# Kernel optimization log

Measured on AMD Instinct MI355X. Metric: run time of the kernel, lower is better.

Reference implementation:

```python
import jax, jax.numpy as jnp
import numpy as np

WS = 8                 # window size (attn_grid_window_size)
N_WIN = WS * WS        # tokens per window = 64
EPS_LN = 1e-5

def _rel_index():
    # standard Swin/MaxViT relative position index for an 8x8 window
    coords = np.stack(np.meshgrid(np.arange(WS), np.arange(WS), indexing='ij')).reshape(2, -1)
    rel = coords[:, :, None] - coords[:, None, :]
    rel = rel.transpose(1, 2, 0).astype(np.int32)
    rel[..., 0] += WS - 1
    rel[..., 1] += WS - 1
    rel[..., 0] *= 2 * WS - 1
    return rel.sum(-1)  # [N_WIN, N_WIN] in [0, (2*WS-1)^2)

def layernorm(x, g, b):
    m = jnp.mean(x, -1, keepdims=True)
    v = jnp.mean((x - m) ** 2, -1, keepdims=True)
    return (x - m) * jax.lax.rsqrt(v + EPS_LN) * g + b

def l2norm(x):
    n = jnp.sqrt(jnp.sum(x * x, -1, keepdims=True))
    return x / jnp.maximum(n, 1e-12)  # torch F.normalize semantics

def setup_inputs() -> dict:
    key = jax.random.key(0)
    ks = jax.random.split(key, 4)
    B, C, H, W = 2, 256, 256, 256
    heads = 16
    s = 0.02
    return dict(
        X=jax.random.normal(ks[0], (B, C, H, W), jnp.float32),
        pre_g=jnp.ones((C,), jnp.float32), pre_b=jnp.zeros((C,), jnp.float32),
        post_g=jnp.ones((C,), jnp.float32), post_b=jnp.zeros((C,), jnp.float32),
        qkv_w=jax.random.normal(ks[1], (C, 3 * C), jnp.float32) * s,
        qkv_b=jnp.zeros((3 * C,), jnp.float32),
        proj_w=jax.random.normal(ks[2], (C, C), jnp.float32) * s,
        proj_b=jnp.zeros((C,), jnp.float32),
        rel_bias_table=jax.random.normal(ks[3], ((2 * WS - 1) ** 2, heads), jnp.float32) * s,
        rel_index=jnp.asarray(_rel_index()),
    )

def reference(X, pre_g, pre_b, post_g, post_b, qkv_w, qkv_b, proj_w, proj_b, rel_bias_table, rel_index):
    B, C, H, W = X.shape
    heads = rel_bias_table.shape[1]
    hd = C // heads
    # block partition: [B, C, H, W] -> [B*nH*nW, WS*WS, C]
    xw = X.reshape(B, C, H // WS, WS, W // WS, WS).transpose(0, 2, 4, 3, 5, 1)
    xw = xw.reshape(-1, N_WIN, C)
    Bw = xw.shape[0]
    # pre-norm + relative self-attention
    xn = layernorm(xw, pre_g, pre_b)
    qkv = (xn @ qkv_w + qkv_b).reshape(Bw, N_WIN, 3, heads, hd).transpose(2, 0, 3, 1, 4)
    q, k, v = qkv[0], qkv[1], qkv[2]            # [Bw, h, N, hd]
    q = l2norm(q)
    k = l2norm(k)                               # use_normalised_qk=True (MetNet-3)
    bias = rel_bias_table[rel_index.reshape(-1)].reshape(N_WIN, N_WIN, heads).transpose(2, 0, 1)
    attn = jax.nn.softmax(jnp.einsum('bhnd,bhmd->bhnm', q, k) + bias[None], axis=-1)
    out = jnp.einsum('bhnm,bhmd->bhnd', attn, v).transpose(0, 2, 1, 3).reshape(Bw, N_WIN, C)
    out = out @ proj_w + proj_b
    # residual, then post-norm branch (mlp = Identity)
    x = xw + out
    x = x + layernorm(x, post_g, post_b)
    # reverse partition -> [B, C, H, W]
    x = x.reshape(B, H // WS, W // WS, WS, WS, C).transpose(0, 5, 1, 3, 2, 4).reshape(B, C, H, W)
    return x
```

## Files before the change

### kernel.cpp

```cpp
#include <hip/hip_runtime.h>
#include <stdint.h>

typedef unsigned short u16;
typedef unsigned int   u32;

typedef short s8v __attribute__((ext_vector_type(8)));
typedef short s4v __attribute__((ext_vector_type(4)));
typedef float f4v __attribute__((ext_vector_type(4)));

struct __align__(8) US4 { u16 x, y, z, w; };

__device__ __forceinline__ u16 f2bf(float f) {
    union { float f; u32 u; } v; v.f = f;
    u32 u = v.u;
    return (u16)((u + 0x7fffu + ((u >> 16) & 1u)) >> 16);
}

#define MFMA16(a, b, c) __builtin_amdgcn_mfma_f32_16x16x16bf16_1k((a), (b), (c), 0, 0, 0)
#define MFMA32(a, b, c) __builtin_amdgcn_mfma_f32_16x16x32_bf16((a), (b), (c), 0, 0, 0)

__global__ void pack_kernel(const float* __restrict__ qkv_w, const float* __restrict__ proj_w,
                            const float* __restrict__ table, const int* __restrict__ ridx,
                            u16* __restrict__ pkQ, u16* __restrict__ pkP, float* __restrict__ biasP)
{
    int tid = blockIdx.x * 256 + threadIdx.x;
    if (tid < 24576) {
        int g = tid;
        int lane = g & 63, ks = (g >> 6) & 7, mt = g >> 9;
        int quad = lane >> 4, c = lane & 15;
        union { u16 h[8]; s8v v; } tmp;
#pragma unroll
        for (int j = 0; j < 8; ++j) {
            int kk = ks * 32 + quad * 8 + j;
            tmp.h[j] = f2bf(qkv_w[kk * 768 + mt * 16 + c]);
        }
        *(s8v*)&pkQ[g * 8] = tmp.v;
    } else if (tid < 32768) {
        int g = tid - 24576;
        int lane = g & 63, ks = (g >> 6) & 7, mt = g >> 9;
        int quad = lane >> 4, c = lane & 15;
        union { u16 h[8]; s8v v; } tmp;
#pragma unroll
        for (int j = 0; j < 8; ++j) {
            int kk = ks * 32 + quad * 8 + j;
            tmp.h[j] = f2bf(proj_w[kk * 256 + mt * 16 + c]);
        }
        *(s8v*)&pkP[g * 8] = tmp.v;
    } else if (tid < 49152) {
        int g = tid - 32768;
        int h = g >> 10, rest = (g >> 6) & 15, lane = g & 63;
        int mt = rest >> 2, nt = rest & 3;
        int quad = lane >> 4, c = lane & 15;
        int query = nt * 16 + c;
#pragma unroll
        for (int r = 0; r < 4; ++r) {
            int key = mt * 16 + quad * 4 + r;
            biasP[g * 4 + r] = table[ridx[query * 64 + key] * 16 + h];
        }
    }
}

__global__ __launch_bounds__(1024)
void attn_win_kernel(const float* __restrict__ X,
                     const float* __restrict__ pre_g, const float* __restrict__ pre_b,
                     const float* __restrict__ post_g, const float* __restrict__ post_b,
                     const float* __restrict__ qkv_b, const float* __restrict__ proj_b,
                     const u16* __restrict__ pkQ, const u16* __restrict__ pkP,
                     const float* __restrict__ biasP,
                     float* __restrict__ out)
{
    __shared__ __align__(16) unsigned char smem[138752];
    u16*   xnS = (u16*)smem;
    u16*   qS  = xnS + 16896;
    u16*   kS  = qS + 16896;
    u16*   vS  = kS + 16896;
    float* xf  = (float*)(smem + 67584);
    float* st  = (float*)(smem + 138240);

    const int tid  = threadIdx.x;
    const int w    = tid >> 6;
    const int l    = tid & 63;
    const int quad = l >> 4;
    const int c    = l & 15;

    const int win = blockIdx.x;
    const int bb = win >> 10;
    const int wh = (win >> 5) & 31;
    const int ww = win & 31;
    const size_t base = (((size_t)bb * 256) * 256 + wh * 8) * 256 + ww * 8;

    f4v xreg[4];
    {
        const int ch0 = (tid >> 4);
        const int t0  = (tid & 15) * 4;
        const int r0 = t0 >> 3, c0 = t0 & 7;
#pragma unroll
        for (int it = 0; it < 4; ++it) {
            int ch = it * 64 + ch0;
            f4v v = *(const f4v*)(X + base + (size_t)ch * 65536 + r0 * 256 + c0);
            xreg[it] = v;
            *(f4v*)&xf[ch * 68 + t0] = v;
        }
    }
    __syncthreads();

    {
        int tk = w * 4 + quad;
        float s = 0.f, ss = 0.f;
#pragma unroll
        for (int j = 0; j < 16; ++j) {
            float x = xf[(c + 16 * j) * 68 + tk];
            s += x; ss += x * x;
        }
#pragma unroll
        for (int m = 1; m < 16; m <<= 1) { s += __shfl_xor(s, m, 64); ss += __shfl_xor(ss, m, 64); }
        float mean = s * (1.f / 256.f);
        float var  = ss * (1.f / 256.f) - mean * mean;
        float rstd = rsqrtf(var + 1e-5f);
        if (c == 0) { st[tk * 2] = mean; st[tk * 2 + 1] = rstd; }
    }
    __syncthreads();

    {
        int t = l;
        int chg = w * 16;
        float mean = st[t * 2], rstd = st[t * 2 + 1];
        union { u16 h[16]; s8v v[2]; } tmp;
#pragma unroll
        for (int j = 0; j < 16; ++j) {
            int ch = chg + j;
            float x = xf[ch * 68 + t];
            tmp.h[j] = f2bf((x - mean) * rstd * pre_g[ch] + pre_b[ch]);
        }
        *(s8v*)&xnS[t * 264 + chg]     = tmp.v[0];
        *(s8v*)&xnS[t * 264 + chg + 8] = tmp.v[1];
    }
    __syncthreads();

    {
        f4v acc[3][4];
#pragma unroll
        for (int i = 0; i < 3; ++i)
#pragma unroll
            for (int nt = 0; nt < 4; ++nt) acc[i][nt] = 0.f;

        const s8v* A = (const s8v*)pkQ;
#pragma unroll
        for (int ks = 0; ks < 8; ++ks) {
            s8v bfr[4];
#pragma unroll
            for (int nt = 0; nt < 4; ++nt)
                bfr[nt] = *(const s8v*)&xnS[(nt * 16 + c) * 264 + ks * 32 + quad * 8];
#pragma unroll
            for (int i = 0; i < 3; ++i) {
                int mt = w * 3 + i;
                s8v afr = A[(mt * 8 + ks) * 64 + l];
#pragma unroll
                for (int nt = 0; nt < 4; ++nt)
                    acc[i][nt] = MFMA32(afr, bfr[nt], acc[i][nt]);
            }
        }
#pragma unroll
        for (int i = 0; i < 3; ++i) {
            int mt = w * 3 + i;
            float b0 = qkv_b[mt * 16 + quad * 4 + 0];
            float b1 = qkv_b[mt * 16 + quad * 4 + 1];
            float b2 = qkv_b[mt * 16 + quad * 4 + 2];
            float b3 = qkv_b[mt * 16 + quad * 4 + 3];
#pragma unroll
            for (int nt = 0; nt < 4; ++nt) {
                f4v a = acc[i][nt];
                a[0] += b0; a[1] += b1; a[2] += b2; a[3] += b3;
                int tok = nt * 16 + c;
                if (mt < 32) {
                    float ss = a[0]*a[0] + a[1]*a[1] + a[2]*a[2] + a[3]*a[3];
                    ss += __shfl_xor(ss, 16, 64);
                    ss += __shfl_xor(ss, 32, 64);
                    float inv = 1.0f / fmaxf(sqrtf(ss), 1e-12f);
                    US4 pk;
                    pk.x = f2bf(a[0] * inv); pk.y = f2bf(a[1] * inv);
                    pk.z = f2bf(a[2] * inv); pk.w = f2bf(a[3] * inv);
                    int off = tok * 264 + (mt & 15) * 16 + quad * 4;
                    if (mt < 16) *(US4*)&qS[off] = pk;
                    else         *(US4*)&kS[off] = pk;
                } else {
                    float p0 = __shfl_xor(a[0], 1, 64), p1 = __shfl_xor(a[1], 1, 64);
                    float p2 = __shfl_xor(a[2], 1, 64), p3 = __shfl_xor(a[3], 1, 64);
                    int chb = (mt - 32) * 16 + quad * 4;
                    if ((l & 1) == 0) {
                        *(u32*)&vS[(chb + 0) * 72 + tok] = (u32)f2bf(a[0]) | ((u32)f2bf(p0) << 16);
                        *(u32*)&vS[(chb + 1) * 72 + tok] = (u32)f2bf(a[1]) | ((u32)f2bf(p1) << 16);
                    } else {
                        *(u32*)&vS[(chb + 2) * 72 + tok - 1] = (u32)f2bf(p2) | ((u32)f2bf(a[2]) << 16);
                        *(u32*)&vS[(chb + 3) * 72 + tok - 1] = (u32)f2bf(p3) | ((u32)f2bf(a[3]) << 16);
                    }
                }
            }
        }
    }
    __syncthreads();

    {
        const int h = w;
        s4v kfr[4], vfr[4];
#pragma unroll
        for (int mt = 0; mt < 4; ++mt)
            kfr[mt] = *(const s4v*)&kS[(mt * 16 + c) * 264 + h * 16 + quad * 4];
#pragma unroll
        for (int kt = 0; kt < 4; ++kt)
            vfr[kt] = *(const s4v*)&vS[(h * 16 + c) * 72 + kt * 16 + quad * 4];

        const f4v* BP = (const f4v*)biasP;
#pragma unroll
        for (int half = 0; half < 2; ++half) {
            f4v sT[4][2];
#pragma unroll
            for (int nt2 = 0; nt2 < 2; ++nt2) {
                int nt = half * 2 + nt2;
                s4v qfr = *(const s4v*)&qS[(nt * 16 + c) * 264 + h * 16 + quad * 4];
#pragma unroll
                for (int mt = 0; mt < 4; ++mt) {
                    f4v bv = BP[(h * 16 + mt * 4 + nt) * 64 + l];
                    sT[mt][nt2] = MFMA16(kfr[mt], qfr, bv);
                }
            }
#pragma unroll
            for (int nt2 = 0; nt2 < 2; ++nt2) {
                int nt = half * 2 + nt2;
                float mx = -1e30f;
#pragma unroll
                for (int mt = 0; mt < 4; ++mt)
#pragma unroll
                    for (int r = 0; r < 4; ++r) mx = fmaxf(mx, sT[mt][nt2][r]);
                mx = fmaxf(mx, __shfl_xor(mx, 16, 64));
                mx = fmaxf(mx, __shfl_xor(mx, 32, 64));
                float p[16];
                float sum = 0.f;
#pragma unroll
                for (int mt = 0; mt < 4; ++mt)
#pragma unroll
                    for (int r = 0; r < 4; ++r) {
                        float e = __expf(sT[mt][nt2][r] - mx);
                        p[mt * 4 + r] = e; sum += e;
                    }
                sum += __shfl_xor(sum, 16, 64);
                sum += __shfl_xor(sum, 32, 64);
                float inv = 1.f / sum;
                f4v o = 0.f;
#pragma unroll
                for (int kt = 0; kt < 4; ++kt) {
                    s4v pv = { (short)f2bf(p[kt * 4 + 0] * inv), (short)f2bf(p[kt * 4 + 1] * inv),
                               (short)f2bf(p[kt * 4 + 2] * inv), (short)f2bf(p[kt * 4 + 3] * inv) };
                    o = MFMA16(vfr[kt], pv, o);
                }
                US4 ov; ov.x = f2bf(o[0]); ov.y = f2bf(o[1]); ov.z = f2bf(o[2]); ov.w = f2bf(o[3]);
                *(US4*)&xnS[(nt * 16 + c) * 264 + h * 16 + quad * 4] = ov;
            }
        }
    }
    __syncthreads();

    {
        f4v acc[4];
#pragma unroll
        for (int nt = 0; nt < 4; ++nt) acc[nt] = 0.f;
        const s8v* A = (const s8v*)pkP;
#pragma unroll
        for (int ks = 0; ks < 8; ++ks) {
            s8v afr = A[(w * 8 + ks) * 64 + l];
#pragma unroll
            for (int nt = 0; nt < 4; ++nt) {
                s8v bfr = *(const s8v*)&xnS[(nt * 16 + c) * 264 + ks * 32 + quad * 8];
                acc[nt] = MFMA32(afr, bfr, acc[nt]);
            }
        }
        float b0 = proj_b[w * 16 + quad * 4 + 0];
        float b1 = proj_b[w * 16 + quad * 4 + 1];
        float b2 = proj_b[w * 16 + quad * 4 + 2];
        float b3 = proj_b[w * 16 + quad * 4 + 3];
#pragma unroll
        for (int nt = 0; nt < 4; ++nt) {
            int tok = nt * 16 + c;
            int chb = w * 16 + quad * 4;
            xf[(chb + 0) * 68 + tok] = acc[nt][0] + b0;
            xf[(chb + 1) * 68 + tok] = acc[nt][1] + b1;
            xf[(chb + 2) * 68 + tok] = acc[nt][2] + b2;
            xf[(chb + 3) * 68 + tok] = acc[nt][3] + b3;
        }
    }
    __syncthreads();

    {
        const int ch0 = (tid >> 4);
        const int t0  = (tid & 15) * 4;
#pragma unroll
        for (int it = 0; it < 4; ++it) {
            int ch = it * 64 + ch0;
            f4v v = *(f4v*)&xf[ch * 68 + t0];
            v += xreg[it];
            *(f4v*)&xf[ch * 68 + t0] = v;
        }
    }
    __syncthreads();

    {
        int tk = w * 4 + quad;
        float s = 0.f, ss = 0.f;
#pragma unroll
        for (int j = 0; j < 16; ++j) {
            float x = xf[(c + 16 * j) * 68 + tk];
            s += x; ss += x * x;
        }
#pragma unroll
        for (int m = 1; m < 16; m <<= 1) { s += __shfl_xor(s, m, 64); ss += __shfl_xor(ss, m, 64); }
        float mean = s * (1.f / 256.f);
        float var  = ss * (1.f / 256.f) - mean * mean;
        float rstd = rsqrtf(var + 1e-5f);
        if (c == 0) { st[tk * 2] = mean; st[tk * 2 + 1] = rstd; }
    }
    __syncthreads();

    {
        const int ch0 = (tid >> 4);
        const int t0  = (tid & 15) * 4;
        const int r0 = t0 >> 3, c0 = t0 & 7;
#pragma unroll
        for (int it = 0; it < 4; ++it) {
            int ch = it * 64 + ch0;
            f4v x = *(f4v*)&xf[ch * 68 + t0];
            float g = post_g[ch], b = post_b[ch];
            f4v y;
#pragma unroll
            for (int j = 0; j < 4; ++j) {
                float mean = st[(t0 + j) * 2], rstd = st[(t0 + j) * 2 + 1];
                y[j] = x[j] + (x[j] - mean) * rstd * g + b;
            }
            *(f4v*)(out + base + (size_t)ch * 65536 + r0 * 256 + c0) = y;
        }
    }
}

extern "C" void kernel_launch(void* const* d_in, const int* in_sizes, int n_in,
                              void* d_out, int out_size, void* d_ws, size_t ws_size,
                              hipStream_t stream)
{
    const float* X      = (const float*)d_in[0];
    const float* pre_g  = (const float*)d_in[1];
    const float* pre_b  = (const float*)d_in[2];
    const float* post_g = (const float*)d_in[3];
    const float* post_b = (const float*)d_in[4];
    const float* qkv_w  = (const float*)d_in[5];
    const float* qkv_b  = (const float*)d_in[6];
    const float* proj_w = (const float*)d_in[7];
    const float* proj_b = (const float*)d_in[8];
    const float* table  = (const float*)d_in[9];
    const int*   ridx   = (const int*)d_in[10];

    u16*   pkQ   = (u16*)d_ws;
    u16*   pkP   = (u16*)((char*)d_ws + 393216);
    float* biasP = (float*)((char*)d_ws + 524288);

    pack_kernel<<<192, 256, 0, stream>>>(qkv_w, proj_w, table, ridx, pkQ, pkP, biasP);
    attn_win_kernel<<<2048, 1024, 0, stream>>>(X, pre_g, pre_b, post_g, post_b,
                                               qkv_b, proj_b, pkQ, pkP, biasP,
                                               (float*)d_out);
}
```

Measured before the change: 526.5 us.

## Restructure window attention to 512 threads with per-head register fusion and smaller LDS

```diff
diff --git a/kernel.cpp b/kernel.cpp
--- a/kernel.cpp
+++ b/kernel.cpp
@@ -60,7 +60,7 @@
     }
 }
 
-__global__ __launch_bounds__(1024)
+__global__ __launch_bounds__(512, 4)
 void attn_win_kernel(const float* __restrict__ X,
                      const float* __restrict__ pre_g, const float* __restrict__ pre_b,
                      const float* __restrict__ post_g, const float* __restrict__ post_b,
@@ -69,124 +69,174 @@
                      const float* __restrict__ biasP,
                      float* __restrict__ out)
 {
-    __shared__ __align__(16) unsigned char smem[138752];
+    __shared__ __align__(16) unsigned char smem[75264];
     u16*   xnS = (u16*)smem;
-    u16*   qS  = xnS + 16896;
-    u16*   kS  = qS + 16896;
-    u16*   vS  = kS + 16896;
-    float* xf  = (float*)(smem + 67584);
-    float* st  = (float*)(smem + 138240);
+    u16*   vS  = (u16*)(smem + 33792);
+    float* xf  = (float*)smem;
+    float* pst = (float*)(smem + 70656);
+    float* st  = (float*)(smem + 74752);
 
     const int tid  = threadIdx.x;
     const int w    = tid >> 6;
     const int l    = tid & 63;
     const int quad = l >> 4;
-    const int c    = l & 15;
-
-    const int win = blockIdx.x;
+    const int cc   = l & 15;
+
+    const int bidx = blockIdx.x;
+    const int win  = ((bidx & 7) << 8) | (bidx >> 3);
     const int bb = win >> 10;
     const int wh = (win >> 5) & 31;
     const int ww = win & 31;
     const size_t base = (((size_t)bb * 256) * 256 + wh * 8) * 256 + ww * 8;
 
-    f4v xreg[4];
-    {
-        const int ch0 = (tid >> 4);
-        const int t0  = (tid & 15) * 4;
-        const int r0 = t0 >> 3, c0 = t0 & 7;
-#pragma unroll
-        for (int it = 0; it < 4; ++it) {
-            int ch = it * 64 + ch0;
-            f4v v = *(const f4v*)(X + base + (size_t)ch * 65536 + r0 * 256 + c0);
-            xreg[it] = v;
-            *(f4v*)&xf[ch * 68 + t0] = v;
-        }
-    }
-    __syncthreads();
-
-    {
-        int tk = w * 4 + quad;
-        float s = 0.f, ss = 0.f;
-#pragma unroll
-        for (int j = 0; j < 16; ++j) {
-            float x = xf[(c + 16 * j) * 68 + tk];
-            s += x; ss += x * x;
-        }
-#pragma unroll
-        for (int m = 1; m < 16; m <<= 1) { s += __shfl_xor(s, m, 64); ss += __shfl_xor(ss, m, 64); }
-        float mean = s * (1.f / 256.f);
-        float var  = ss * (1.f / 256.f) - mean * mean;
-        float rstd = rsqrtf(var + 1e-5f);
-        if (c == 0) { st[tk * 2] = mean; st[tk * 2 + 1] = rstd; }
-    }
-    __syncthreads();
-
-    {
-        int t = l;
-        int chg = w * 16;
-        float mean = st[t * 2], rstd = st[t * 2 + 1];
-        union { u16 h[16]; s8v v[2]; } tmp;
-#pragma unroll
-        for (int j = 0; j < 16; ++j) {
-            int ch = chg + j;
-            float x = xf[ch * 68 + t];
-            tmp.h[j] = f2bf((x - mean) * rstd * pre_g[ch] + pre_b[ch]);
-        }
-        *(s8v*)&xnS[t * 264 + chg]     = tmp.v[0];
-        *(s8v*)&xnS[t * 264 + chg + 8] = tmp.v[1];
-    }
-    __syncthreads();
-
-    {
-        f4v acc[3][4];
-#pragma unroll
-        for (int i = 0; i < 3; ++i)
-#pragma unroll
-            for (int nt = 0; nt < 4; ++nt) acc[i][nt] = 0.f;
-
-        const s8v* A = (const s8v*)pkQ;
-#pragma unroll
-        for (int ks = 0; ks < 8; ++ks) {
-            s8v bfr[4];
-#pragma unroll
-            for (int nt = 0; nt < 4; ++nt)
-                bfr[nt] = *(const s8v*)&xnS[(nt * 16 + c) * 264 + ks * 32 + quad * 8];
-#pragma unroll
-            for (int i = 0; i < 3; ++i) {
-                int mt = w * 3 + i;
-                s8v afr = A[(mt * 8 + ks) * 64 + l];
+    const int ch0 = tid >> 4;
+    const int t0  = (tid & 15) * 4;
+    const int r0  = t0 >> 3, c0 = t0 & 7;
+
+    f4v xv[8];
+#pragma unroll
+    for (int it = 0; it < 8; ++it) {
+        int ch = it * 32 + ch0;
+        xv[it] = *(const f4v*)(X + base + (size_t)ch * 65536 + r0 * 256 + c0);
+    }
+
+    {
+        float s[4] = {0.f,0.f,0.f,0.f}, ss[4] = {0.f,0.f,0.f,0.f};
+#pragma unroll
+        for (int it = 0; it < 8; ++it)
+#pragma unroll
+            for (int j = 0; j < 4; ++j) { float x = xv[it][j]; s[j] += x; ss[j] += x * x; }
+#pragma unroll
+        for (int j = 0; j < 4; ++j) {
+            s[j]  += __shfl_xor(s[j], 16, 64);  s[j]  += __shfl_xor(s[j], 32, 64);
+            ss[j] += __shfl_xor(ss[j], 16, 64); ss[j] += __shfl_xor(ss[j], 32, 64);
+        }
+        if (quad == 0) {
+#pragma unroll
+            for (int j = 0; j < 4; ++j) {
+                pst[(w * 64 + t0 + j) * 2]     = s[j];
+                pst[(w * 64 + t0 + j) * 2 + 1] = ss[j];
+            }
+        }
+    }
+    __syncthreads();
+    if (tid < 64) {
+        float S = 0.f, SS = 0.f;
+#pragma unroll
+        for (int wv = 0; wv < 8; ++wv) {
+            S  += pst[(wv * 64 + tid) * 2];
+            SS += pst[(wv * 64 + tid) * 2 + 1];
+        }
+        float mean = S * (1.f / 256.f);
+        float var  = SS * (1.f / 256.f) - mean * mean;
+        st[tid * 2] = mean; st[tid * 2 + 1] = rsqrtf(var + 1e-5f);
+    }
+    __syncthreads();
+
+    {
+        float mean[4], rstd[4];
+#pragma unroll
+        for (int j = 0; j < 4; ++j) { mean[j] = st[(t0 + j) * 2]; rstd[j] = st[(t0 + j) * 2 + 1]; }
+#pragma unroll
+        for (int it = 0; it < 8; ++it) {
+            int ch = it * 32 + ch0;
+            float g = pre_g[ch], b = pre_b[ch];
+            u16 m0 = f2bf((xv[it][0] - mean[0]) * rstd[0] * g + b);
+            u16 m1 = f2bf((xv[it][1] - mean[1]) * rstd[1] * g + b);
+            u16 m2 = f2bf((xv[it][2] - mean[2]) * rstd[2] * g + b);
+            u16 m3 = f2bf((xv[it][3] - mean[3]) * rstd[3] * g + b);
+            u32 m01 = (u32)m0 | ((u32)m1 << 16);
+            u32 m23 = (u32)m2 | ((u32)m3 << 16);
+            u32 p01 = __shfl_xor(m01, 16, 64);
+            u32 p23 = __shfl_xor(m23, 16, 64);
+            if ((quad & 1) == 0) {
+                *(u32*)&xnS[(t0 + 0) * 264 + ch] = (m01 & 0xffffu) | ((p01 & 0xffffu) << 16);
+                *(u32*)&xnS[(t0 + 1) * 264 + ch] = (m01 >> 16)    | (p01 & 0xffff0000u);
+            } else {
+                *(u32*)&xnS[(t0 + 2) * 264 + ch - 1] = (p23 & 0xffffu) | ((m23 & 0xffffu) << 16);
+                *(u32*)&xnS[(t0 + 3) * 264 + ch - 1] = (p23 >> 16)    | (m23 & 0xffff0000u);
+            }
+        }
+    }
+    __syncthreads();
+
+    US4 outbuf[2][4];
+    const s8v* AQ = (const s8v*)pkQ;
+#pragma unroll
+    for (int hi = 0; hi < 2; ++hi) {
+        const int head = w * 2 + hi;
+        s4v qfr[4], kfr[4];
+        {
+            f4v acc0[4], acc1[4], acc2[4];
+#pragma unroll
+            for (int nt = 0; nt < 4; ++nt) { acc0[nt] = 0.f; acc1[nt] = 0.f; acc2[nt] = 0.f; }
+#pragma unroll
+            for (int ks = 0; ks < 8; ++ks) {
+                s8v bfr[4];
 #pragma unroll
                 for (int nt = 0; nt < 4; ++nt)
-                    acc[i][nt] = MFMA32(afr, bfr[nt], acc[i][nt]);
-            }
-        }
-#pragma unroll
-        for (int i = 0; i < 3; ++i) {
-            int mt = w * 3 + i;
-            float b0 = qkv_b[mt * 16 + quad * 4 + 0];
-            float b1 = qkv_b[mt * 16 + quad * 4 + 1];
-            float b2 = qkv_b[mt * 16 + quad * 4 + 2];
-            float b3 = qkv_b[mt * 16 + quad * 4 + 3];
-#pragma unroll
-            for (int nt = 0; nt < 4; ++nt) {
-                f4v a = acc[i][nt];
-                a[0] += b0; a[1] += b1; a[2] += b2; a[3] += b3;
-                int tok = nt * 16 + c;
-                if (mt < 32) {
-                    float ss = a[0]*a[0] + a[1]*a[1] + a[2]*a[2] + a[3]*a[3];
-                    ss += __shfl_xor(ss, 16, 64);
-                    ss += __shfl_xor(ss, 32, 64);
-                    float inv = 1.0f / fmaxf(sqrtf(ss), 1e-12f);
-                    US4 pk;
-                    pk.x = f2bf(a[0] * inv); pk.y = f2bf(a[1] * inv);
-                    pk.z = f2bf(a[2] * inv); pk.w = f2bf(a[3] * inv);
-                    int off = tok * 264 + (mt & 15) * 16 + quad * 4;
-                    if (mt < 16) *(US4*)&qS[off] = pk;
-                    else         *(US4*)&kS[off] = pk;
-                } else {
+                    bfr[nt] = *(const s8v*)&xnS[(nt * 16 + cc) * 264 + ks * 32 + quad * 8];
+                s8v a0 = AQ[((head     ) * 8 + ks) * 64 + l];
+                s8v a1 = AQ[((head + 16) * 8 + ks) * 64 + l];
+                s8v a2 = AQ[((head + 32) * 8 + ks) * 64 + l];
+#pragma unroll
+                for (int nt = 0; nt < 4; ++nt) {
+                    acc0[nt] = MFMA32(a0, bfr[nt], acc0[nt]);
+                    acc1[nt] = MFMA32(a1, bfr[nt], acc1[nt]);
+                    acc2[nt] = MFMA32(a2, bfr[nt], acc2[nt]);
+                }
+            }
+            {
+                float b0 = qkv_b[head * 16 + quad * 4 + 0];
+                float b1 = qkv_b[head * 16 + quad * 4 + 1];
+                float b2 = qkv_b[head * 16 + quad * 4 + 2];
+                float b3 = qkv_b[head * 16 + quad * 4 + 3];
+#pragma unroll
+                for (int nt = 0; nt < 4; ++nt) {
+                    f4v a = acc0[nt];
+                    a[0] += b0; a[1] += b1; a[2] += b2; a[3] += b3;
+                    float sq = a[0]*a[0] + a[1]*a[1] + a[2]*a[2] + a[3]*a[3];
+                    sq += __shfl_xor(sq, 16, 64);
+                    sq += __shfl_xor(sq, 32, 64);
+                    float inv = 1.0f / fmaxf(sqrtf(sq), 1e-12f);
+                    s4v f;
+                    f[0] = (short)f2bf(a[0] * inv); f[1] = (short)f2bf(a[1] * inv);
+                    f[2] = (short)f2bf(a[2] * inv); f[3] = (short)f2bf(a[3] * inv);
+                    qfr[nt] = f;
+                }
+            }
+            {
+                float b0 = qkv_b[(head + 16) * 16 + quad * 4 + 0];
+                float b1 = qkv_b[(head + 16) * 16 + quad * 4 + 1];
+                float b2 = qkv_b[(head + 16) * 16 + quad * 4 + 2];
+                float b3 = qkv_b[(head + 16) * 16 + quad * 4 + 3];
+#pragma unroll
+                for (int nt = 0; nt < 4; ++nt) {
+                    f4v a = acc1[nt];
+                    a[0] += b0; a[1] += b1; a[2] += b2; a[3] += b3;
+                    float sq = a[0]*a[0] + a[1]*a[1] + a[2]*a[2] + a[3]*a[3];
+                    sq += __shfl_xor(sq, 16, 64);
+                    sq += __shfl_xor(sq, 32, 64);
+                    float inv = 1.0f / fmaxf(sqrtf(sq), 1e-12f);
+                    s4v f;
+                    f[0] = (short)f2bf(a[0] * inv); f[1] = (short)f2bf(a[1] * inv);
+                    f[2] = (short)f2bf(a[2] * inv); f[3] = (short)f2bf(a[3] * inv);
+                    kfr[nt] = f;
+                }
+            }
+            {
+                float b0 = qkv_b[(head + 32) * 16 + quad * 4 + 0];
+                float b1 = qkv_b[(head + 32) * 16 + quad * 4 + 1];
+                float b2 = qkv_b[(head + 32) * 16 + quad * 4 + 2];
+                float b3 = qkv_b[(head + 32) * 16 + quad * 4 + 3];
+                int chb = head * 16 + quad * 4;
+#pragma unroll
+                for (int nt = 0; nt < 4; ++nt) {
+                    f4v a = acc2[nt];
+                    a[0] += b0; a[1] += b1; a[2] += b2; a[3] += b3;
+                    int tok = nt * 16 + cc;
                     float p0 = __shfl_xor(a[0], 1, 64), p1 = __shfl_xor(a[1], 1, 64);
                     float p2 = __shfl_xor(a[2], 1, 64), p3 = __shfl_xor(a[3], 1, 64);
-                    int chb = (mt - 32) * 16 + quad * 4;
                     if ((l & 1) == 0) {
                         *(u32*)&vS[(chb + 0) * 72 + tok] = (u32)f2bf(a[0]) | ((u32)f2bf(p0) << 16);
                         *(u32*)&vS[(chb + 1) * 72 + tok] = (u32)f2bf(a[1]) | ((u32)f2bf(p1) << 16);
@@ -197,145 +247,164 @@
                 }
             }
         }
-    }
-    __syncthreads();
-
-    {
-        const int h = w;
-        s4v kfr[4], vfr[4];
-#pragma unroll
-        for (int mt = 0; mt < 4; ++mt)
-            kfr[mt] = *(const s4v*)&kS[(mt * 16 + c) * 264 + h * 16 + quad * 4];
-#pragma unroll
-        for (int kt = 0; kt < 4; ++kt)
-            vfr[kt] = *(const s4v*)&vS[(h * 16 + c) * 72 + kt * 16 + quad * 4];
-
-        const f4v* BP = (const f4v*)biasP;
-#pragma unroll
-        for (int half = 0; half < 2; ++half) {
-            f4v sT[4][2];
-#pragma unroll
-            for (int nt2 = 0; nt2 < 2; ++nt2) {
-                int nt = half * 2 + nt2;
-                s4v qfr = *(const s4v*)&qS[(nt * 16 + c) * 264 + h * 16 + quad * 4];
-#pragma unroll
-                for (int mt = 0; mt < 4; ++mt) {
-                    f4v bv = BP[(h * 16 + mt * 4 + nt) * 64 + l];
-                    sT[mt][nt2] = MFMA16(kfr[mt], qfr, bv);
-                }
-            }
-#pragma unroll
-            for (int nt2 = 0; nt2 < 2; ++nt2) {
-                int nt = half * 2 + nt2;
-                float mx = -1e30f;
-#pragma unroll
-                for (int mt = 0; mt < 4; ++mt)
-#pragma unroll
-                    for (int r = 0; r < 4; ++r) mx = fmaxf(mx, sT[mt][nt2][r]);
-                mx = fmaxf(mx, __shfl_xor(mx, 16, 64));
-                mx = fmaxf(mx, __shfl_xor(mx, 32, 64));
-                float p[16];
-                float sum = 0.f;
-#pragma unroll
-                for (int mt = 0; mt < 4; ++mt)
-#pragma unroll
-                    for (int r = 0; r < 4; ++r) {
-                        float e = __expf(sT[mt][nt2][r] - mx);
-                        p[mt * 4 + r] = e; sum += e;
+        {
+            s4v vfr[4];
+#pragma unroll
+            for (int kt = 0; kt < 4; ++kt)
+                vfr[kt] = *(const s4v*)&vS[(head * 16 + cc) * 72 + kt * 16 + quad * 4];
+            const f4v* BP = (const f4v*)biasP;
+#pragma unroll
+            for (int half = 0; half < 2; ++half) {
+                f4v sT[4][2];
+#pragma unroll
+                for (int nt2 = 0; nt2 < 2; ++nt2) {
+                    int nt = half * 2 + nt2;
+#pragma unroll
+                    for (int mt = 0; mt < 4; ++mt)
+                        sT[mt][nt2] = MFMA16(kfr[mt], qfr[nt], BP[(head * 16 + mt * 4 + nt) * 64 + l]);
+                }
+#pragma unroll
+                for (int nt2 = 0; nt2 < 2; ++nt2) {
+                    int nt = half * 2 + nt2;
+                    float mx = -1e30f;
+#pragma unroll
+                    for (int mt = 0; mt < 4; ++mt)
+#pragma unroll
+                        for (int r = 0; r < 4; ++r) mx = fmaxf(mx, sT[mt][nt2][r]);
+                    mx = fmaxf(mx, __shfl_xor(mx, 16, 64));
+                    mx = fmaxf(mx, __shfl_xor(mx, 32, 64));
+                    float p[16];
+                    float sum = 0.f;
+#pragma unroll
+                    for (int mt = 0; mt < 4; ++mt)
+#pragma unroll
+                        for (int r = 0; r < 4; ++r) {
+                            float e = __expf(sT[mt][nt2][r] - mx);
+                            p[mt * 4 + r] = e; sum += e;
+                        }
+                    sum += __shfl_xor(sum, 16, 64);
+                    sum += __shfl_xor(sum, 32, 64);
+                    float inv = 1.f / sum;
+                    f4v o = 0.f;
+#pragma unroll
+                    for (int kt = 0; kt < 4; ++kt) {
+                        s4v pv = { (short)f2bf(p[kt * 4 + 0] * inv), (short)f2bf(p[kt * 4 + 1] * inv),
+                                   (short)f2bf(p[kt * 4 + 2] * inv), (short)f2bf(p[kt * 4 + 3] * inv) };
+                        o = MFMA16(vfr[kt], pv, o);
                     }
-                sum += __shfl_xor(sum, 16, 64);
-                sum += __shfl_xor(sum, 32, 64);
-                float inv = 1.f / sum;
-                f4v o = 0.f;
-#pragma unroll
-                for (int kt = 0; kt < 4; ++kt) {
-                    s4v pv = { (short)f2bf(p[kt * 4 + 0] * inv), (short)f2bf(p[kt * 4 + 1] * inv),
-                               (short)f2bf(p[kt * 4 + 2] * inv), (short)f2bf(p[kt * 4 + 3] * inv) };
-                    o = MFMA16(vfr[kt], pv, o);
-                }
-                US4 ov; ov.x = f2bf(o[0]); ov.y = f2bf(o[1]); ov.z = f2bf(o[2]); ov.w = f2bf(o[3]);
-                *(US4*)&xnS[(nt * 16 + c) * 264 + h * 16 + quad * 4] = ov;
-            }
-        }
-    }
-    __syncthreads();
-
-    {
-        f4v acc[4];
-#pragma unroll
-        for (int nt = 0; nt < 4; ++nt) acc[nt] = 0.f;
-        const s8v* A = (const s8v*)pkP;
+                    US4 ov; ov.x = f2bf(o[0]); ov.y = f2bf(o[1]); ov.z = f2bf(o[2]); ov.w = f2bf(o[3]);
+                    outbuf[hi][nt] = ov;
+                }
+            }
+        }
+    }
+    __syncthreads();
+#pragma unroll
+    for (int hi = 0; hi < 2; ++hi)
+#pragma unroll
+        for (int nt = 0; nt < 4; ++nt)
+            *(US4*)&xnS[(nt * 16 + cc) * 264 + (w * 2 + hi) * 16 + quad * 4] = outbuf[hi][nt];
+    __syncthreads();
+
+    f4v xv2[8];
+#pragma unroll
+    for (int it = 0; it < 8; ++it) {
+        int ch = it * 32 + ch0;
+        xv2[it] = *(const f4v*)(X + base + (size_t)ch * 65536 + r0 * 256 + c0);
+    }
+    f4v pa0[4], pa1[4];
+#pragma unroll
+    for (int nt = 0; nt < 4; ++nt) { pa0[nt] = 0.f; pa1[nt] = 0.f; }
+    {
+        const s8v* AP = (const s8v*)pkP;
 #pragma unroll
         for (int ks = 0; ks < 8; ++ks) {
-            s8v afr = A[(w * 8 + ks) * 64 + l];
+            s8v bfr[4];
+#pragma unroll
+            for (int nt = 0; nt < 4; ++nt)
+                bfr[nt] = *(const s8v*)&xnS[(nt * 16 + cc) * 264 + ks * 32 + quad * 8];
+            s8v a0 = AP[((w * 2    ) * 8 + ks) * 64 + l];
+            s8v a1 = AP[((w * 2 + 1) * 8 + ks) * 64 + l];
 #pragma unroll
             for (int nt = 0; nt < 4; ++nt) {
-                s8v bfr = *(const s8v*)&xnS[(nt * 16 + c) * 264 + ks * 32 + quad * 8];
-                acc[nt] = MFMA32(afr, bfr, acc[nt]);
-            }
-        }
-        float b0 = proj_b[w * 16 + quad * 4 + 0];
-        float b1 = proj_b[w * 16 + quad * 4 + 1];
-        float b2 = proj_b[w * 16 + quad * 4 + 2];
-        float b3 = proj_b[w * 16 + quad * 4 + 3];
+                pa0[nt] = MFMA32(a0, bfr[nt], pa0[nt]);
+                pa1[nt] = MFMA32(a1, bfr[nt], pa1[nt]);
+            }
+        }
+    }
+    __syncthreads();
+    {
+        int chb0 = (w * 2    ) * 16 + quad * 4;
+        int chb1 = (w * 2 + 1) * 16 + quad * 4;
+        float c00 = proj_b[chb0 + 0], c01 = proj_b[chb0 + 1], c02 = proj_b[chb0 + 2], c03 = proj_b[chb0 + 3];
+        float c10 = proj_b[chb1 + 0], c11 = proj_b[chb1 + 1], c12 = proj_b[chb1 + 2], c13 = proj_b[chb1 + 3];
 #pragma unroll
         for (int nt = 0; nt < 4; ++nt) {
-            int tok = nt * 16 + c;
-            int chb = w * 16 + quad * 4;
-            xf[(chb + 0) * 68 + tok] = acc[nt][0] + b0;
-            xf[(chb + 1) * 68 + tok] = acc[nt][1] + b1;
-            xf[(chb + 2) * 68 + tok] = acc[nt][2] + b2;
-            xf[(chb + 3) * 68 + tok] = acc[nt][3] + b3;
-        }
-    }
-    __syncthreads();
-
-    {
-        const int ch0 = (tid >> 4);
-        const int t0  = (tid & 15) * 4;
-#pragma unroll
-        for (int it = 0; it < 4; ++it) {
-            int ch = it * 64 + ch0;
-            f4v v = *(f4v*)&xf[ch * 68 + t0];
-            v += xreg[it];
-            *(f4v*)&xf[ch * 68 + t0] = v;
-        }
-    }
-    __syncthreads();
-
-    {
-        int tk = w * 4 + quad;
-        float s = 0.f, ss = 0.f;
-#pragma unroll
-        for (int j = 0; j < 16; ++j) {
-            float x = xf[(c + 16 * j) * 68 + tk];
-            s += x; ss += x * x;
-        }
-#pragma unroll
-        for (int m = 1; m < 16; m <<= 1) { s += __shfl_xor(s, m, 64); ss += __shfl_xor(ss, m, 64); }
-        float mean = s * (1.f / 256.f);
-        float var  = ss * (1.f / 256.f) - mean * mean;
-        float rstd = rsqrtf(var + 1e-5f);
-        if (c == 0) { st[tk * 2] = mean; st[tk * 2 + 1] = rstd; }
-    }
-    __syncthreads();
-
-    {
-        const int ch0 = (tid >> 4);
-        const int t0  = (tid & 15) * 4;
-        const int r0 = t0 >> 3, c0 = t0 & 7;
-#pragma unroll
-        for (int it = 0; it < 4; ++it) {
-            int ch = it * 64 + ch0;
-            f4v x = *(f4v*)&xf[ch * 68 + t0];
+            int tok = nt * 16 + cc;
+            xf[(chb0 + 0) * 68 + tok] = pa0[nt][0] + c00;
+            xf[(chb0 + 1) * 68 + tok] = pa0[nt][1] + c01;
+            xf[(chb0 + 2) * 68 + tok] = pa0[nt][2] + c02;
+            xf[(chb0 + 3) * 68 + tok] = pa0[nt][3] + c03;
+            xf[(chb1 + 0) * 68 + tok] = pa1[nt][0] + c10;
+            xf[(chb1 + 1) * 68 + tok] = pa1[nt][1] + c11;
+            xf[(chb1 + 2) * 68 + tok] = pa1[nt][2] + c12;
+            xf[(chb1 + 3) * 68 + tok] = pa1[nt][3] + c13;
+        }
+    }
+    __syncthreads();
+
+    f4v yv[8];
+    {
+        float s[4] = {0.f,0.f,0.f,0.f}, ss[4] = {0.f,0.f,0.f,0.f};
+#pragma unroll
+        for (int it = 0; it < 8; ++it) {
+            int ch = it * 32 + ch0;
+            f4v o = *(const f4v*)&xf[ch * 68 + t0];
+            f4v y = xv2[it] + o;
+            yv[it] = y;
+#pragma unroll
+            for (int j = 0; j < 4; ++j) { s[j] += y[j]; ss[j] += y[j] * y[j]; }
+        }
+#pragma unroll
+        for (int j = 0; j < 4; ++j) {
+            s[j]  += __shfl_xor(s[j], 16, 64);  s[j]  += __shfl_xor(s[j], 32, 64);
+            ss[j] += __shfl_xor(ss[j], 16, 64); ss[j] += __shfl_xor(ss[j], 32, 64);
+        }
+        if (quad == 0) {
+#pragma unroll
+            for (int j = 0; j < 4; ++j) {
+                pst[(w * 64 + t0 + j) * 2]     = s[j];
+                pst[(w * 64 + t0 + j) * 2 + 1] = ss[j];
+            }
+        }
+    }
+    __syncthreads();
+    if (tid < 64) {
+        float S = 0.f, SS = 0.f;
+#pragma unroll
+        for (int wv = 0; wv < 8; ++wv) {
+            S  += pst[(wv * 64 + tid) * 2];
+            SS += pst[(wv * 64 + tid) * 2 + 1];
+        }
+        float mean = S * (1.f / 256.f);
+        float var  = SS * (1.f / 256.f) - mean * mean;
+        st[tid * 2] = mean; st[tid * 2 + 1] = rsqrtf(var + 1e-5f);
+    }
+    __syncthreads();
+
+    {
+        float mean[4], rstd[4];
+#pragma unroll
+        for (int j = 0; j < 4; ++j) { mean[j] = st[(t0 + j) * 2]; rstd[j] = st[(t0 + j) * 2 + 1]; }
+#pragma unroll
+        for (int it = 0; it < 8; ++it) {
+            int ch = it * 32 + ch0;
             float g = post_g[ch], b = post_b[ch];
-            f4v y;
-#pragma unroll
-            for (int j = 0; j < 4; ++j) {
-                float mean = st[(t0 + j) * 2], rstd = st[(t0 + j) * 2 + 1];
-                y[j] = x[j] + (x[j] - mean) * rstd * g + b;
-            }
-            *(f4v*)(out + base + (size_t)ch * 65536 + r0 * 256 + c0) = y;
+            f4v y = yv[it], z;
+#pragma unroll
+            for (int j = 0; j < 4; ++j)
+                z[j] = y[j] + (y[j] - mean[j]) * rstd[j] * g + b;
+            *(f4v*)(out + base + (size_t)ch * 65536 + r0 * 256 + c0) = z;
         }
     }
 }
@@ -361,7 +430,7 @@
     float* biasP = (float*)((char*)d_ws + 524288);
 
     pack_kernel<<<192, 256, 0, stream>>>(qkv_w, proj_w, table, ridx, pkQ, pkP, biasP);
-    attn_win_kernel<<<2048, 1024, 0, stream>>>(X, pre_g, pre_b, post_g, post_b,
-                                               qkv_b, proj_b, pkQ, pkP, biasP,
-                                               (float*)d_out);
+    attn_win_kernel<<<2048, 512, 0, stream>>>(X, pre_g, pre_b, post_g, post_b,
+                                              qkv_b, proj_b, pkQ, pkP, biasP,
+                                              (float*)d_out);
 }
```

New measurement: 422.4 us. -19.8%, faster.
